# Optimization experiments

Hardware: AMD Instinct MI355X
Metric: run time of the kernel (lower is better)

## Reference

```python
import jax, jax.numpy as jnp
import numpy as np

_SHAPE = (4, 2, 8, 256, 513)  # N, 2(real/imag), C, T, F


def setup_inputs() -> dict:
    key = jax.random.key(0)
    k1, k2, k3 = jax.random.split(key, 3)
    return {
        "mixture": jax.random.normal(k1, _SHAPE, dtype=jnp.float32),
        "target": jax.random.normal(k2, _SHAPE, dtype=jnp.float32),
        "noise": jax.random.normal(k3, _SHAPE, dtype=jnp.float32),
        "ref_mic_idx": 0,
    }


def _to_complex(x):
    # (N, 2, C, T, F) real-imag stacked -> complex (N, C, T, F)
    return jax.lax.complex(x[:, 0], x[:, 1])


def _mean_spatial_cov(s):
    # s: complex (N, C, T, F) -> time-averaged covariance (N, F, C, C)
    N, C, T, F = s.shape
    sc = jnp.transpose(s, (0, 3, 2, 1))  # (N, F, T, C)
    # outer product V V^H summed over T, fused into one batched GEMM
    return jnp.einsum("nftc,nftd->nfcd", sc, jnp.conj(sc)) / T


def reference(mixture, target, noise, ref_mic_idx):
    y = _to_complex(mixture)  # (N, C, T, F)
    x = _to_complex(target)
    v = _to_complex(noise)
    N, C, T, F = y.shape

    phi_target = _mean_spatial_cov(x)  # (N, F, C, C)
    # diagonal loading: torch adds load to BOTH real and imag parts (RI dim broadcast)
    load = (0.001 / np.sqrt(2)) * (1.0 + 1.0j)
    phi_noise = _mean_spatial_cov(v) + jnp.asarray(load, dtype=y.dtype) * jnp.eye(C, dtype=y.dtype)

    G = jnp.linalg.inv(phi_noise) @ phi_target  # (N, F, C, C)
    l = jnp.trace(G, axis1=-2, axis2=-1)  # (N, F)
    # W = (1/l) * G @ e_ref  -> select column ref_mic_idx
    W = G[..., ref_mic_idx] / l[..., None]  # (N, F, C)

    # X_bf(n,t,f) = W^H y = sum_c conj(W)_{nfc} y_{nctf}
    X_bf = jnp.einsum("nfc,nctf->ntf", jnp.conj(W), y)  # (N, T, F)
    # restack real/imag and add singleton channel dim -> (N, 2, 1, T, F)
    out = jnp.stack([X_bf.real, X_bf.imag], axis=1)[:, :, None]
    return out
```

## Files before the change

### kernel.cpp

```cpp
#include <hip/hip_runtime.h>

#define Nn 4
#define Cc 8
#define Tt 256
#define Ff 513
#define TFs (Tt * Ff)
#define NCHUNK 16
#define TCHUNK (Tt / NCHUNK)
#define SLAB ((size_t)Ff * 72)

template <int G>
__device__ __forceinline__ void cov_group(const float* __restrict__ bt,
                                          float (*red)[73], int lane)
{
    constexpr int R2 = 7 - G;
    float ar[9], ai[9];
#pragma unroll
    for (int s = 0; s < 9; ++s) { ar[s] = 0.f; ai[s] = 0.f; }

#pragma unroll 2
    for (int tt = 0; tt < TCHUNK; ++tt) {
        float re[8], im[8];
#pragma unroll
        for (int c = G; c < 8; ++c) {
            re[c] = bt[(size_t)c * TFs];
            im[c] = bt[(size_t)(Cc + c) * TFs];
        }
        int s = 0;
#pragma unroll
        for (int d = G; d < 8; ++d, ++s) {
            ar[s] += re[G] * re[d] + im[G] * im[d];
            if (d != G) ai[s] += im[G] * re[d] - re[G] * im[d];
        }
#pragma unroll
        for (int d = R2; d < 8; ++d, ++s) {
            ar[s] += re[R2] * re[d] + im[R2] * im[d];
            if (d != R2) ai[s] += im[R2] * re[d] - re[R2] * im[d];
        }
        bt += Ff;
    }

    int s = 0;
#pragma unroll
    for (int d = G; d < 8; ++d, ++s) {
        const int p = G * 8 - G * (G - 1) / 2 + (d - G);
        red[lane][2 * p]     = ar[s];
        red[lane][2 * p + 1] = (d == G) ? 0.f : ai[s];
    }
#pragma unroll
    for (int d = R2; d < 8; ++d, ++s) {
        const int p = R2 * 8 - R2 * (R2 - 1) / 2 + (d - R2);
        red[lane][2 * p]     = ar[s];
        red[lane][2 * p + 1] = (d == R2) ? 0.f : ai[s];
    }
}

__global__ __launch_bounds__(256) void cov_partial(
    const float* __restrict__ target, const float* __restrict__ noise,
    float* __restrict__ partial)
{
    int tid = threadIdx.x;
    int lane = tid & 63, wave = tid >> 6;
    int f0 = blockIdx.x * 64;
    int f = f0 + lane;
    int fc = f < Ff ? f : (Ff - 1);
    int n = blockIdx.y;
    int z = blockIdx.z;
    int inp = z & 1;
    int chunk = z >> 1;

    const float* src = inp ? noise : target;
    const float* bt = src + (size_t)n * 2 * Cc * TFs
                      + (size_t)(chunk * TCHUNK) * Ff + fc;

    __shared__ float red[64][73];
    switch (wave) {
        case 0: cov_group<0>(bt, red, lane); break;
        case 1: cov_group<1>(bt, red, lane); break;
        case 2: cov_group<2>(bt, red, lane); break;
        default: cov_group<3>(bt, red, lane); break;
    }
    __syncthreads();

    int nf = Ff - f0; if (nf > 64) nf = 64;
    float* dst = partial + (((size_t)inp * Nn + n) * NCHUNK + chunk) * SLAB
                 + (size_t)f0 * 72;
    for (int i = tid; i < nf * 72; i += 256) {
        int fl = i / 72, j = i - fl * 72;
        dst[i] = red[fl][j];
    }
}

__global__ __launch_bounds__(64) void mvdr_weights(
    const float* __restrict__ partial, const int* __restrict__ ref_ptr,
    float2* __restrict__ wconj)
{
    int f = blockIdx.x;
    int n = blockIdx.y;
    int lane = threadIdx.x;

    int r = lane >> 3, c = lane & 7;
    int lo = r < c ? r : c, hi = r < c ? c : r;
    int p = lo * 8 - lo * (lo - 1) / 2 + (hi - lo);

    const float* pT = partial + ((size_t)(0 * Nn + n) * NCHUNK) * SLAB
                      + (size_t)f * 72 + 2 * p;
    const float* pN = partial + ((size_t)(1 * Nn + n) * NCHUNK) * SLAB
                      + (size_t)f * 72 + 2 * p;
    float2 sT = make_float2(0.f, 0.f), sN = make_float2(0.f, 0.f);
#pragma unroll
    for (int ch = 0; ch < NCHUNK; ++ch) {
        float2 vT = *(const float2*)(pT + ch * SLAB);
        float2 vN = *(const float2*)(pN + ch * SLAB);
        sT.x += vT.x; sT.y += vT.y;
        sN.x += vN.x; sN.y += vN.y;
    }

    const float invT = 1.0f / (float)Tt;
    const float dl = 0.001f / 1.41421356237309515f;
    float sgn = (r > c) ? -1.f : 1.f;

    float2 a = make_float2(sN.x * invT, sgn * sN.y * invT);
    float2 b = make_float2(sT.x * invT, sgn * sT.y * invT);
    if (r == c) { a.x += dl; a.y += dl; }

    for (int k = 0; k < 8; ++k) {
        float mag = (c == k && r >= k) ? (a.x * a.x + a.y * a.y) : -1.f;
        int midx = r;
#pragma unroll
        for (int st = 8; st < 64; st <<= 1) {
            float om = __shfl_xor(mag, st, 64);
            int   oi = __shfl_xor(midx, st, 64);
            if (om > mag) { mag = om; midx = oi; }
        }
        int piv = __shfl(midx, k, 64);

        int srcr = (r == k) ? piv : ((r == piv) ? k : r);
        int src = srcr * 8 + c;
        a.x = __shfl(a.x, src, 64); a.y = __shfl(a.y, src, 64);
        b.x = __shfl(b.x, src, 64); b.y = __shfl(b.y, src, 64);

        float pvx = __shfl(a.x, k * 8 + k, 64), pvy = __shfl(a.y, k * 8 + k, 64);
        float d = pvx * pvx + pvy * pvy;
        float ipx = pvx / d, ipy = -pvy / d;
        if (r == k) {
            float2 t = a;
            a = make_float2(t.x * ipx - t.y * ipy, t.x * ipy + t.y * ipx);
            t = b;
            b = make_float2(t.x * ipx - t.y * ipy, t.x * ipy + t.y * ipx);
        }

        float rax = __shfl(a.x, k * 8 + c, 64), ray = __shfl(a.y, k * 8 + c, 64);
        float rbx = __shfl(b.x, k * 8 + c, 64), rby = __shfl(b.y, k * 8 + c, 64);
        float fx  = __shfl(a.x, r * 8 + k, 64), fy  = __shfl(a.y, r * 8 + k, 64);
        if (r != k) {
            a.x -= fx * rax - fy * ray;  a.y -= fx * ray + fy * rax;
            b.x -= fx * rbx - fy * rby;  b.y -= fx * rby + fy * rbx;
        }
    }

    float tx = (r == c) ? b.x : 0.f, ty = (r == c) ? b.y : 0.f;
#pragma unroll
    for (int st = 1; st < 64; st <<= 1) {
        tx += __shfl_xor(tx, st, 64);
        ty += __shfl_xor(ty, st, 64);
    }

    int ref = *ref_ptr;
    if (c == ref) {
        float den = tx * tx + ty * ty;
        float wx = (b.x * tx + b.y * ty) / den;
        float wy = (b.y * tx - b.x * ty) / den;
        wconj[((size_t)n * Ff + f) * 8 + r] = make_float2(wx, -wy);
    }
}

__global__ __launch_bounds__(256) void beamform(
    const float* __restrict__ y, const float2* __restrict__ wconj,
    float* __restrict__ out)
{
    int idx = blockIdx.x * 256 + threadIdx.x;
    int n = idx / TFs;
    int rem = idx - n * TFs;
    int t = rem / Ff;
    int f = rem - t * Ff;

    size_t base_re = (size_t)n * 2 * Cc * TFs + (size_t)t * Ff + f;
    size_t base_im = base_re + (size_t)Cc * TFs;
    const float2* w = wconj + ((size_t)n * Ff + f) * 8;

    float xr = 0.f, xi = 0.f;
#pragma unroll
    for (int c = 0; c < Cc; ++c) {
        float yre = y[base_re + (size_t)c * TFs];
        float yim = y[base_im + (size_t)c * TFs];
        float2 wc = w[c];
        xr += wc.x * yre - wc.y * yim;
        xi += wc.x * yim + wc.y * yre;
    }
    size_t ob = (size_t)n * 2 * TFs + (size_t)t * Ff + f;
    out[ob] = xr;
    out[ob + TFs] = xi;
}

extern "C" void kernel_launch(void* const* d_in, const int* in_sizes, int n_in,
                              void* d_out, int out_size, void* d_ws, size_t ws_size,
                              hipStream_t stream) {
    const float* mixture = (const float*)d_in[0];
    const float* target  = (const float*)d_in[1];
    const float* noise   = (const float*)d_in[2];
    const int*   refp    = (const int*)d_in[3];
    float* out = (float*)d_out;

    float*  partial = (float*)d_ws;
    float2* wconj = (float2*)((char*)d_ws +
                              (size_t)2 * Nn * NCHUNK * SLAB * sizeof(float));

    cov_partial<<<dim3(9, Nn, NCHUNK * 2), 256, 0, stream>>>(target, noise, partial);
    mvdr_weights<<<dim3(Ff, Nn), 64, 0, stream>>>(partial, refp, wconj);
    beamform<<<dim3((Nn * TFs) / 256), 256, 0, stream>>>(mixture, wconj, out);
}
```

Before: 156.8 us.

## Share channel loads across waves via double-buffered LDS in covariance kernel

```diff
diff --git a/kernel.cpp b/kernel.cpp
--- a/kernel.cpp
+++ b/kernel.cpp
@@ -9,37 +9,90 @@
 #define TCHUNK (Tt / NCHUNK)
 #define SLAB ((size_t)Ff * 72)
 
+
+#define ROWS(Rbase, chan, j) ((Rbase) + (((chan) * 2 + (j)) * 64))
+
 template <int G>
-__device__ __forceinline__ void cov_group(const float* __restrict__ bt,
-                                          float (*red)[73], int lane)
+__device__ __forceinline__ void cov_wave(const float* __restrict__ base,
+                                         float* __restrict__ smem, int lane)
 {
     constexpr int R2 = 7 - G;
+    float* buf0 = smem;
+    float* buf1 = smem + 2048;
+
     float ar[9], ai[9];
 #pragma unroll
     for (int s = 0; s < 9; ++s) { ar[s] = 0.f; ai[s] = 0.f; }
 
-#pragma unroll 2
-    for (int tt = 0; tt < TCHUNK; ++tt) {
-        float re[8], im[8];
-#pragma unroll
-        for (int c = G; c < 8; ++c) {
-            re[c] = bt[(size_t)c * TFs];
-            im[c] = bt[(size_t)(Cc + c) * TFs];
-        }
-        int s = 0;
-#pragma unroll
-        for (int d = G; d < 8; ++d, ++s) {
-            ar[s] += re[G] * re[d] + im[G] * im[d];
-            if (d != G) ai[s] += im[G] * re[d] - re[G] * im[d];
-        }
-#pragma unroll
-        for (int d = R2; d < 8; ++d, ++s) {
-            ar[s] += re[R2] * re[d] + im[R2] * im[d];
-            if (d != R2) ai[s] += im[R2] * re[d] - re[R2] * im[d];
-        }
-        bt += Ff;
-    }
-
+    const float* g0 = base + (size_t)(4 * G + 0) * TFs;
+    const float* g1 = base + (size_t)(4 * G + 1) * TFs;
+    const float* g2 = base + (size_t)(4 * G + 2) * TFs;
+    const float* g3 = base + (size_t)(4 * G + 3) * TFs;
+
+#define ACCUM_PAIR(R)                                                         \
+    do {                                                                      \
+        _Pragma("unroll")                                                     \
+        for (int j = 0; j < 2; ++j) {                                         \
+            float re[8], im[8];                                               \
+            _Pragma("unroll")                                                 \
+            for (int c2 = G; c2 < 8; ++c2) {                                  \
+                re[c2] = ROWS(R, c2, j)[lane];                                \
+                im[c2] = ROWS(R, 8 + c2, j)[lane];                            \
+            }                                                                 \
+            int s = 0;                                                        \
+            _Pragma("unroll")                                                 \
+            for (int d = G; d < 8; ++d, ++s) {                                \
+                ar[s] += re[G] * re[d] + im[G] * im[d];                       \
+                if (d != G) ai[s] += im[G] * re[d] - re[G] * im[d];           \
+            }                                                                 \
+            _Pragma("unroll")                                                 \
+            for (int d = R2; d < 8; ++d, ++s) {                               \
+                ar[s] += re[R2] * re[d] + im[R2] * im[d];                     \
+                if (d != R2) ai[s] += im[R2] * re[d] - re[R2] * im[d];        \
+            }                                                                 \
+        }                                                                     \
+    } while (0)
+
+    {
+        float a0 = g0[0], b0 = g0[Ff], a1 = g1[0], b1 = g1[Ff];
+        float a2 = g2[0], b2 = g2[Ff], a3 = g3[0], b3 = g3[Ff];
+        g0 += 2 * Ff; g1 += 2 * Ff; g2 += 2 * Ff; g3 += 2 * Ff;
+        ROWS(buf0, 4 * G + 0, 0)[lane] = a0; ROWS(buf0, 4 * G + 0, 1)[lane] = b0;
+        ROWS(buf0, 4 * G + 1, 0)[lane] = a1; ROWS(buf0, 4 * G + 1, 1)[lane] = b1;
+        ROWS(buf0, 4 * G + 2, 0)[lane] = a2; ROWS(buf0, 4 * G + 2, 1)[lane] = b2;
+        ROWS(buf0, 4 * G + 3, 0)[lane] = a3; ROWS(buf0, 4 * G + 3, 1)[lane] = b3;
+    }
+
+    for (int ph = 0; ph < 8; ph += 2) {
+        __syncthreads();
+        {
+            float a0 = g0[0], b0 = g0[Ff], a1 = g1[0], b1 = g1[Ff];
+            float a2 = g2[0], b2 = g2[Ff], a3 = g3[0], b3 = g3[Ff];
+            g0 += 2 * Ff; g1 += 2 * Ff; g2 += 2 * Ff; g3 += 2 * Ff;
+            ACCUM_PAIR(buf0);
+            ROWS(buf1, 4 * G + 0, 0)[lane] = a0; ROWS(buf1, 4 * G + 0, 1)[lane] = b0;
+            ROWS(buf1, 4 * G + 1, 0)[lane] = a1; ROWS(buf1, 4 * G + 1, 1)[lane] = b1;
+            ROWS(buf1, 4 * G + 2, 0)[lane] = a2; ROWS(buf1, 4 * G + 2, 1)[lane] = b2;
+            ROWS(buf1, 4 * G + 3, 0)[lane] = a3; ROWS(buf1, 4 * G + 3, 1)[lane] = b3;
+        }
+        __syncthreads();
+        if (ph < 6) {
+            float a0 = g0[0], b0 = g0[Ff], a1 = g1[0], b1 = g1[Ff];
+            float a2 = g2[0], b2 = g2[Ff], a3 = g3[0], b3 = g3[Ff];
+            g0 += 2 * Ff; g1 += 2 * Ff; g2 += 2 * Ff; g3 += 2 * Ff;
+            ACCUM_PAIR(buf1);
+            ROWS(buf0, 4 * G + 0, 0)[lane] = a0; ROWS(buf0, 4 * G + 0, 1)[lane] = b0;
+            ROWS(buf0, 4 * G + 1, 0)[lane] = a1; ROWS(buf0, 4 * G + 1, 1)[lane] = b1;
+            ROWS(buf0, 4 * G + 2, 0)[lane] = a2; ROWS(buf0, 4 * G + 2, 1)[lane] = b2;
+            ROWS(buf0, 4 * G + 3, 0)[lane] = a3; ROWS(buf0, 4 * G + 3, 1)[lane] = b3;
+        } else {
+            ACCUM_PAIR(buf1);
+        }
+    }
+#undef ACCUM_PAIR
+
+    __syncthreads();
+    float (*red)[73] = (float(*)[73])smem;
     int s = 0;
 #pragma unroll
     for (int d = G; d < 8; ++d, ++s) {
@@ -55,7 +108,7 @@
     }
 }
 
-__global__ __launch_bounds__(256) void cov_partial(
+__global__ __launch_bounds__(256, 8) void cov_partial(
     const float* __restrict__ target, const float* __restrict__ noise,
     float* __restrict__ partial)
 {
@@ -70,19 +123,20 @@
     int chunk = z >> 1;
 
     const float* src = inp ? noise : target;
-    const float* bt = src + (size_t)n * 2 * Cc * TFs
-                      + (size_t)(chunk * TCHUNK) * Ff + fc;
-
-    __shared__ float red[64][73];
+    const float* base = src + (size_t)n * 2 * Cc * TFs
+                        + (size_t)(chunk * TCHUNK) * Ff + fc;
+
+    __shared__ float smem[64 * 73];
     switch (wave) {
-        case 0: cov_group<0>(bt, red, lane); break;
-        case 1: cov_group<1>(bt, red, lane); break;
-        case 2: cov_group<2>(bt, red, lane); break;
-        default: cov_group<3>(bt, red, lane); break;
+        case 0: cov_wave<0>(base, smem, lane); break;
+        case 1: cov_wave<1>(base, smem, lane); break;
+        case 2: cov_wave<2>(base, smem, lane); break;
+        default: cov_wave<3>(base, smem, lane); break;
     }
     __syncthreads();
 
     int nf = Ff - f0; if (nf > 64) nf = 64;
+    float (*red)[73] = (float(*)[73])smem;
     float* dst = partial + (((size_t)inp * Nn + n) * NCHUNK + chunk) * SLAB
                  + (size_t)f0 * 72;
     for (int i = tid; i < nf * 72; i += 256) {
```

New measurement: 150.8 us. 1.04x faster.
